# Performance work log

Hardware: AMD Instinct MI355X
Metric: run time of the kernel (lower is better)

The kernel has to match this reference:

```python
import jax, jax.numpy as jnp
import numpy as np

B, C, HW = 128, 3, 224
P = 16
D = 256
NH = 8
HD = D // NH
E = 4            # num_experts
K = 2            # top-k
FF = 4 * D
NC = 38
EPS = 1e-5


def _layernorm(x, g, b):
    mu = jnp.mean(x, axis=-1, keepdims=True)
    var = jnp.mean(jnp.square(x - mu), axis=-1, keepdims=True)
    return (x - mu) * jax.lax.rsqrt(var + EPS) * g + b


def setup_inputs() -> dict:
    key = jax.random.key(0)
    ks = jax.random.split(key, 16)
    s = 0.02
    return {
        "x": jax.random.normal(ks[0], (B, C, HW, HW), dtype=jnp.float32),
        "conv_w": jax.random.normal(ks[1], (D, C, P, P), dtype=jnp.float32) * s,
        "conv_b": jnp.zeros((D,), jnp.float32),
        "cls_token": jnp.zeros((1, 1, D), jnp.float32),
        "ln1_g": jnp.ones((D,), jnp.float32),
        "ln1_b": jnp.zeros((D,), jnp.float32),
        "qkv_w": jax.random.normal(ks[2], (3 * D, D), dtype=jnp.float32) * s,
        "qkv_b": jnp.zeros((3 * D,), jnp.float32),
        "out_w": jax.random.normal(ks[3], (D, D), dtype=jnp.float32) * s,
        "out_b": jnp.zeros((D,), jnp.float32),
        "ln2_g": jnp.ones((D,), jnp.float32),
        "ln2_b": jnp.zeros((D,), jnp.float32),
        "router_w": jax.random.normal(ks[4], (E, D), dtype=jnp.float32) * s,
        "router_b": jnp.zeros((E,), jnp.float32),
        "e_w1": jax.random.normal(ks[5], (E, D, FF), dtype=jnp.float32) * s,
        "e_b1": jnp.zeros((E, FF), jnp.float32),
        "e_w2": jax.random.normal(ks[6], (E, FF, D), dtype=jnp.float32) * s,
        "e_b2": jnp.zeros((E, D), jnp.float32),
        "head_w": jax.random.normal(ks[7], (NC, D), dtype=jnp.float32) * s,
        "head_b": jnp.zeros((NC,), jnp.float32),
    }


def reference(x, conv_w, conv_b, cls_token, ln1_g, ln1_b, qkv_w, qkv_b,
              out_w, out_b, ln2_g, ln2_b, router_w, router_b,
              e_w1, e_b1, e_w2, e_b2, head_w, head_b):
    # patch embed: Conv2d(3, D, 16, 16) -> [B, D, 14, 14] -> [B, 196, D]
    h = jax.lax.conv_general_dilated(
        x, conv_w, window_strides=(P, P), padding="VALID",
        dimension_numbers=("NCHW", "OIHW", "NCHW")) + conv_b[None, :, None, None]
    b = h.shape[0]
    tok = h.reshape(b, D, -1).transpose(0, 2, 1)            # [B, 196, D]
    tok = jnp.concatenate([jnp.broadcast_to(cls_token, (b, 1, D)), tok], axis=1)  # [B, 197, D]
    S = tok.shape[1]

    # Multi-head self-attention (pre-norm)
    x2 = _layernorm(tok, ln1_g, ln1_b)
    qkv = x2 @ qkv_w.T + qkv_b                              # [B, S, 3D]
    q, k, v = jnp.split(qkv, 3, axis=-1)
    q = q.reshape(b, S, NH, HD)
    k = k.reshape(b, S, NH, HD)
    v = v.reshape(b, S, NH, HD)
    scores = jnp.einsum("bqhd,bkhd->bhqk", q, k) / np.float32(np.sqrt(HD))
    attn = jax.nn.softmax(scores, axis=-1)
    ao = jnp.einsum("bhqk,bkhd->bqhd", attn, v).reshape(b, S, D)
    ao = ao @ out_w.T + out_b
    tok = tok + ao

    # MoE FFN (pre-norm). NOTE: original code computes top-k routing weights
    # but never multiplies outputs by them — outputs of selected experts are
    # simply summed. We reproduce that faithfully.
    x2 = _layernorm(tok, ln2_g, ln2_b)
    x_flat = x2.reshape(-1, D)                              # [T, D]
    logits = x_flat @ router_w.T + router_b                 # [T, E]
    probs = jax.nn.softmax(logits, axis=-1)
    _topw, topi = jax.lax.top_k(probs, K)                   # topw unused (as in source)
    mask = (topi[..., None] == jnp.arange(E)).any(axis=1)   # [T, E] bool
    out_flat = jnp.zeros_like(x_flat)
    for i in range(E):                                       # fixed small expert count
        hid = jax.nn.gelu(x_flat @ e_w1[i] + e_b1[i], approximate=False)
        out_flat = out_flat + mask[:, i:i + 1].astype(x_flat.dtype) * (hid @ e_w2[i] + e_b2[i])
    tok = tok + out_flat.reshape(b, S, D)

    return tok[:, 0] @ head_w.T + head_b                    # [B, NC]
```

## Files before the change

### kernel.cpp

```cpp
#include <hip/hip_runtime.h>
#include <hip/hip_bf16.h>
#include <math.h>

#define TTOK   25216
#define SEQL   197
#define NBATCH 128
#define DMODEL 256
#define NHEADS 8
#define FFD    1024
#define NEXP   4
#define NCLS   38
#define CONVK  768
#define NPATCH 196
#define CM     25088

typedef unsigned short u16;
typedef unsigned int u32;
using s16x8 = __attribute__((ext_vector_type(8))) short;
using f32x4 = __attribute__((ext_vector_type(4))) float;

__device__ __forceinline__ float b2f(u16 v) {
  union { unsigned u; float f; } x; x.u = (unsigned)v << 16; return x.f;
}
__device__ __forceinline__ u16 f2b(float f) {
  __hip_bfloat16 h = __float2bfloat16(f);
  return *reinterpret_cast<u16*>(&h);
}
__device__ __forceinline__ void gload16(const void* g, void* l) {
  __builtin_amdgcn_global_load_lds(
      (const __attribute__((address_space(1))) void*)g,
      (__attribute__((address_space(3))) void*)l, 16, 0, 0);
}
__device__ __forceinline__ float warp_sum(float v) {
  #pragma unroll
  for (int o = 32; o; o >>= 1) v += __shfl_xor(v, o);
  return v;
}
__device__ __forceinline__ float warp_max(float v) {
  #pragma unroll
  for (int o = 32; o; o >>= 1) v = fmaxf(v, __shfl_xor(v, o));
  return v;
}
__device__ __forceinline__ int fsw(int row) { return (row ^ (row >> 2)) & 3; }

__global__ __launch_bounds__(256) void k_cast2(const float* __restrict__ in,
                                               u16* __restrict__ hi,
                                               u16* __restrict__ lo) {
  int i = (blockIdx.x * 256 + threadIdx.x) * 4;
  float4 v = *(const float4*)&in[i];
  float vv[4] = {v.x, v.y, v.z, v.w};
  u16 h[4], l[4];
  #pragma unroll
  for (int j = 0; j < 4; ++j) {
    h[j] = f2b(vv[j]);
    l[j] = f2b(vv[j] - b2f(h[j]));
  }
  *(uint2*)&hi[i] = *(const uint2*)h;
  *(uint2*)&lo[i] = *(const uint2*)l;
}

__global__ __launch_bounds__(256) void k_conv(const float* __restrict__ x,
                                              const u16* __restrict__ cwh,
                                              const u16* __restrict__ cwl,
                                              const float* __restrict__ cb,
                                              float* __restrict__ tok) {
  const int m0 = blockIdx.x * 128;
  const int n0 = blockIdx.y * 128;
  __shared__ __align__(16) u16 lds[4 * 128 * 32];
  u16* Ah_s = lds;
  u16* Al_s = lds + 4096;
  u16* Wh_s = lds + 8192;
  u16* Wl_s = lds + 12288;
  const int tid = threadIdx.x;
  const int lane = tid & 63;
  const int wv = tid >> 6;
  const int wr = wv >> 1, wc = wv & 1;
  const int l15 = lane & 15, l4 = lane >> 4;
  f32x4 acc[4][4] = {};

  const int kk_t = (tid & 7) * 4;
  long abase[4]; int aldso[4];
  #pragma unroll
  for (int it = 0; it < 4; ++it) {
    int row = it * 32 + (tid >> 3);
    int m = m0 + row;
    int b = m / NPATCH, p = m - b * NPATCH;
    int py = p / 14, px = p - py * 14;
    abase[it] = (long)(b * 3) * 50176 + (py * 16) * 224 + px * 16;
    aldso[it] = row * 64 + (((kk_t >> 3) ^ fsw(row)) << 4) + (kk_t & 7) * 2;
  }
  long woff[2]; int wofs[2];
  #pragma unroll
  for (int r = 0; r < 2; ++r) {
    int off = r * 4096 + tid * 16;
    int row = off >> 6;
    int c16 = (off >> 4) & 3;
    int kk = (c16 ^ fsw(row)) << 3;
    woff[r] = (long)(n0 + row) * CONVK + kk;
    wofs[r] = off;
  }
  for (int kc = 0; kc < CONVK; kc += 32) {
    #pragma unroll
    for (int r = 0; r < 2; ++r) {
      gload16(cwh + woff[r] + kc, (char*)Wh_s + wofs[r]);
      gload16(cwl + woff[r] + kc, (char*)Wl_s + wofs[r]);
    }
    int k = kc + kk_t;
    int c = k >> 8, r8 = k & 255;
    long soff = (long)c * 50176 + (r8 >> 4) * 224 + (r8 & 15);
    #pragma unroll
    for (int it = 0; it < 4; ++it) {
      float4 v = *(const float4*)&x[abase[it] + soff];
      float vv[4] = {v.x, v.y, v.z, v.w};
      u16 h[4], l[4];
      #pragma unroll
      for (int j = 0; j < 4; ++j) {
        h[j] = f2b(vv[j]);
        l[j] = f2b(vv[j] - b2f(h[j]));
      }
      *(uint2*)((char*)Ah_s + aldso[it]) = *(const uint2*)h;
      *(uint2*)((char*)Al_s + aldso[it]) = *(const uint2*)l;
    }
    __syncthreads();
    s16x8 ah[4], al[4], bh[4], bl[4];
    #pragma unroll
    for (int i = 0; i < 4; ++i) {
      int rowa = wr * 64 + i * 16 + l15;
      int kba = (l4 ^ fsw(rowa)) << 4;
      ah[i] = *(const s16x8*)((const char*)Ah_s + rowa * 64 + kba);
      al[i] = *(const s16x8*)((const char*)Al_s + rowa * 64 + kba);
      int rowb = wc * 64 + i * 16 + l15;
      int kbb = (l4 ^ fsw(rowb)) << 4;
      bh[i] = *(const s16x8*)((const char*)Wh_s + rowb * 64 + kbb);
      bl[i] = *(const s16x8*)((const char*)Wl_s + rowb * 64 + kbb);
    }
    #pragma unroll
    for (int i = 0; i < 4; ++i)
      #pragma unroll
      for (int j = 0; j < 4; ++j)
        acc[i][j] = __builtin_amdgcn_mfma_f32_16x16x32_bf16(ah[i], bh[j],
                                                            acc[i][j], 0, 0, 0);
    #pragma unroll
    for (int i = 0; i < 4; ++i)
      #pragma unroll
      for (int j = 0; j < 4; ++j)
        acc[i][j] = __builtin_amdgcn_mfma_f32_16x16x32_bf16(ah[i], bl[j],
                                                            acc[i][j], 0, 0, 0);
    #pragma unroll
    for (int i = 0; i < 4; ++i)
      #pragma unroll
      for (int j = 0; j < 4; ++j)
        acc[i][j] = __builtin_amdgcn_mfma_f32_16x16x32_bf16(al[i], bh[j],
                                                            acc[i][j], 0, 0, 0);
    __syncthreads();
  }
  const int mb = m0 + wr * 64 + (l4 << 2);
  const int nb = n0 + wc * 64 + l15;
  #pragma unroll
  for (int i = 0; i < 4; ++i) {
    #pragma unroll
    for (int jf = 0; jf < 4; ++jf) {
      #pragma unroll
      for (int j = 0; j < 4; ++j) {
        int m = mb + i * 16 + j;
        int n = nb + jf * 16;
        int bq = m / NPATCH;
        long cr = (long)bq * SEQL + (m - bq * NPATCH) + 1;
        tok[cr * DMODEL + n] = acc[i][jf][j] + cb[n];
      }
    }
  }
}

__global__ __launch_bounds__(256) void k_qkv(const u16* __restrict__ Ah,
                                             const u16* __restrict__ Al,
                                             const u16* __restrict__ Wh,
                                             const u16* __restrict__ Wl,
                                             const float* __restrict__ bias,
                                             float* __restrict__ Cf) {
  const int m0 = blockIdx.x * 128;
  const int n0 = blockIdx.y * 128;
  const int K = DMODEL, ldc = 512;
  __shared__ __align__(16) u16 lds[4 * 128 * 32];
  u16* Ah_s = lds;
  u16* Al_s = lds + 4096;
  u16* Wh_s = lds + 8192;
  u16* Wl_s = lds + 12288;
  const int tid = threadIdx.x;
  const int lane = tid & 63;
  const int wv = tid >> 6;
  const int wr = wv >> 1, wc = wv & 1;
  const int l15 = lane & 15, l4 = lane >> 4;
  f32x4 acc[4][4] = {};

  long aoff[2], woff[2]; int ofs[2];
  #pragma unroll
  for (int r = 0; r < 2; ++r) {
    int off = r * 4096 + tid * 16;
    int row = off >> 6;
    int c16 = (off >> 4) & 3;
    int kk = (c16 ^ fsw(row)) << 3;
    aoff[r] = (long)(m0 + row) * K + kk;
    woff[r] = (long)(n0 + row) * K + kk;
    ofs[r] = off;
  }
  for (int kc = 0; kc < K; kc += 32) {
    #pragma unroll
    for (int r = 0; r < 2; ++r) {
      gload16(Ah + aoff[r] + kc, (char*)Ah_s + ofs[r]);
      gload16(Al + aoff[r] + kc, (char*)Al_s + ofs[r]);
      gload16(Wh + woff[r] + kc, (char*)Wh_s + ofs[r]);
      gload16(Wl + woff[r] + kc, (char*)Wl_s + ofs[r]);
    }
    __syncthreads();
    s16x8 ah[4], al[4], bh[4], bl[4];
    #pragma unroll
    for (int i = 0; i < 4; ++i) {
      int rowa = wr * 64 + i * 16 + l15;
      int kba = (l4 ^ fsw(rowa)) << 4;
      ah[i] = *(const s16x8*)((const char*)Ah_s + rowa * 64 + kba);
      al[i] = *(const s16x8*)((const char*)Al_s + rowa * 64 + kba);
      int rowb = wc * 64 + i * 16 + l15;
      int kbb = (l4 ^ fsw(rowb)) << 4;
      bh[i] = *(const s16x8*)((const char*)Wh_s + rowb * 64 + kbb);
      bl[i] = *(const s16x8*)((const char*)Wl_s + rowb * 64 + kbb);
    }
    #pragma unroll
    for (int i = 0; i < 4; ++i)
      #pragma unroll
      for (int j = 0; j < 4; ++j)
        acc[i][j] = __builtin_amdgcn_mfma_f32_16x16x32_bf16(ah[i], bh[j],
                                                            acc[i][j], 0, 0, 0);
    #pragma unroll
    for (int i = 0; i < 4; ++i)
      #pragma unroll
      for (int j = 0; j < 4; ++j)
        acc[i][j] = __builtin_amdgcn_mfma_f32_16x16x32_bf16(ah[i], bl[j],
                                                            acc[i][j], 0, 0, 0);
    #pragma unroll
    for (int i = 0; i < 4; ++i)
      #pragma unroll
      for (int j = 0; j < 4; ++j)
        acc[i][j] = __builtin_amdgcn_mfma_f32_16x16x32_bf16(al[i], bh[j],
                                                            acc[i][j], 0, 0, 0);
    __syncthreads();
  }
  const int mb = m0 + wr * 64 + (l4 << 2);
  const int nb = n0 + wc * 64 + l15;
  #pragma unroll
  for (int i = 0; i < 4; ++i) {
    #pragma unroll
    for (int jf = 0; jf < 4; ++jf) {
      #pragma unroll
      for (int j = 0; j < 4; ++j) {
        int m = mb + i * 16 + j;
        int n = nb + jf * 16;
        Cf[(long)m * ldc + n] = acc[i][jf][j] + bias[n];
      }
    }
  }
}

__global__ __launch_bounds__(256) void k_ln4(const float* __restrict__ in,
                                             u16* __restrict__ outh,
                                             u16* __restrict__ outl,
                                             const float* __restrict__ g,
                                             const float* __restrict__ bb) {
  const int row = blockIdx.x * 4 + (threadIdx.x >> 6);
  const int lane = threadIdx.x & 63;
  float vv[4];
  *(float4*)vv = *(const float4*)&in[(size_t)row * DMODEL + lane * 4];
  float s1 = vv[0] + vv[1] + vv[2] + vv[3];
  float s2 = vv[0]*vv[0] + vv[1]*vv[1] + vv[2]*vv[2] + vv[3]*vv[3];
  s1 = warp_sum(s1);
  s2 = warp_sum(s2);
  float mu = s1 * (1.f / DMODEL);
  float var = s2 * (1.f / DMODEL) - mu * mu;
  float rs = rsqrtf(var + 1e-5f);
  u16 hh[4], ll[4];
  #pragma unroll
  for (int j = 0; j < 4; ++j) {
    float r = (vv[j] - mu) * rs * g[lane * 4 + j] + bb[lane * 4 + j];
    hh[j] = f2b(r);
    ll[j] = f2b(r - b2f(hh[j]));
  }
  *(uint2*)&outh[(size_t)row * DMODEL + lane * 4] = *(const uint2*)hh;
  *(uint2*)&outl[(size_t)row * DMODEL + lane * 4] = *(const uint2*)ll;
}

__global__ void k_cls(const float* __restrict__ cls, float* __restrict__ tok) {
  tok[(size_t)blockIdx.x * SEQL * DMODEL + threadIdx.x] = cls[threadIdx.x];
}

__global__ __launch_bounds__(256) void k_qcls(const u16* __restrict__ x2h,
                                              const u16* __restrict__ x2l,
                                              const u16* __restrict__ qwh,
                                              const u16* __restrict__ qwl,
                                              const float* __restrict__ qb,
                                              u16* __restrict__ qch,
                                              u16* __restrict__ qcl) {
  const int b = blockIdx.x, n = threadIdx.x;
  __shared__ float xs[DMODEL];
  size_t r0 = (size_t)b * SEQL * DMODEL;
  xs[n] = b2f(x2h[r0 + n]) + b2f(x2l[r0 + n]);
  __syncthreads();
  float val = qb[n];
  #pragma unroll 4
  for (int i = 0; i < 32; ++i) {
    s16x8 wh = *(const s16x8*)(qwh + (size_t)n * DMODEL + i * 8);
    s16x8 wl = *(const s16x8*)(qwl + (size_t)n * DMODEL + i * 8);
    #pragma unroll
    for (int j = 0; j < 8; ++j)
      val = fmaf(b2f((u16)wh[j]) + b2f((u16)wl[j]), xs[i * 8 + j], val);
  }
  u16 h = f2b(val);
  qch[b * DMODEL + n] = h;
  qcl[b * DMODEL + n] = f2b(val - b2f(h));
}

__global__ __launch_bounds__(256) void k_attn_cls(const u16* __restrict__ qch,
                                                  const u16* __restrict__ qcl,
                                                  const float* __restrict__ kvf,
                                                  float* __restrict__ ao) {
  const int w = threadIdx.x >> 6, lane = threadIdx.x & 63;
  const int unit = blockIdx.x * 4 + w;
  const int b = unit >> 3, h = unit & 7;
  __shared__ float Ss[4][200];
  float q[32];
  #pragma unroll
  for (int i = 0; i < 4; ++i) {
    s16x8 vh = *(const s16x8*)(qch + b * DMODEL + h * 32 + i * 8);
    s16x8 vl = *(const s16x8*)(qcl + b * DMODEL + h * 32 + i * 8);
    #pragma unroll
    for (int j = 0; j < 8; ++j) q[i * 8 + j] = b2f((u16)vh[j]) + b2f((u16)vl[j]);
  }
  float sc[4];
  float mx = -1e30f;
  #pragma unroll
  for (int r = 0; r < 4; ++r) {
    int k = lane + 64 * r;
    float s = -1e30f;
    if (k < SEQL) {
      const float* kr = kvf + ((size_t)(b * SEQL + k)) * 512 + h * 32;
      s = 0.f;
      #pragma unroll
      for (int i = 0; i < 8; ++i) {
        float4 kv4 = *(const float4*)(kr + i * 4);
        s = fmaf(kv4.x, q[i * 4 + 0], s);
        s = fmaf(kv4.y, q[i * 4 + 1], s);
        s = fmaf(kv4.z, q[i * 4 + 2], s);
        s = fmaf(kv4.w, q[i * 4 + 3], s);
      }
      s *= 0.17677669529663687f;
    }
    sc[r] = s;
    mx = fmaxf(mx, s);
  }
  mx = warp_max(mx);
  float sm = 0.f;
  #pragma unroll
  for (int r = 0; r < 4; ++r) {
    int k = lane + 64 * r;
    float e = (k < SEQL) ? __expf(sc[r] - mx) : 0.f;
    sc[r] = e;
    sm += e;
  }
  sm = warp_sum(sm);
  float inv = 1.f / sm;
  #pragma unroll
  for (int r = 0; r < 4; ++r) {
    int k = lane + 64 * r;
    if (k < SEQL) Ss[w][k] = sc[r] * inv;
  }
  int d = lane & 31, half = lane >> 5;
  float acc = 0.f;
  for (int i = 0; i < 99; ++i) {
    int k = half * 99 + i;
    if (k < SEQL)
      acc = fmaf(Ss[w][k], kvf[((size_t)(b * SEQL + k)) * 512 + 256 + h * 32 + d], acc);
  }
  acc += __shfl_xor(acc, 32);
  if (lane < 32) ao[(b * NHEADS + h) * 32 + d] = acc;
}

__global__ __launch_bounds__(256) void k_oproj_route(
    const float* __restrict__ ao, const float* __restrict__ ow,
    const float* __restrict__ ob, const float* __restrict__ tok,
    const float* __restrict__ g, const float* __restrict__ bb,
    const float* __restrict__ rw, const float* __restrict__ rb,
    float* __restrict__ tokc, float* __restrict__ x2cf,
    float* __restrict__ maskf) {
  const int b = blockIdx.x, n = threadIdx.x;
  const int w = n >> 6, lane = n & 63;
  __shared__ float xs[DMODEL];
  __shared__ float xd_s[DMODEL];
  __shared__ float red[8];
  __shared__ float lg[4];
  xs[n] = ao[b * DMODEL + n];
  __syncthreads();
  float val = ob[n];
  #pragma unroll 4
  for (int i = 0; i < 64; ++i) {
    float4 wv = *(const float4*)(ow + (size_t)n * DMODEL + i * 4);
    val = fmaf(wv.x, xs[i * 4 + 0], val);
    val = fmaf(wv.y, xs[i * 4 + 1], val);
    val = fmaf(wv.z, xs[i * 4 + 2], val);
    val = fmaf(wv.w, xs[i * 4 + 3], val);
  }
  float t = tok[(size_t)b * SEQL * DMODEL + n] + val;
  tokc[b * DMODEL + n] = t;
  float s1 = warp_sum(t), s2 = warp_sum(t * t);
  if (lane == 0) { red[w] = s1; red[4 + w] = s2; }
  __syncthreads();
  s1 = red[0] + red[1] + red[2] + red[3];
  s2 = red[4] + red[5] + red[6] + red[7];
  float mu = s1 * (1.f / DMODEL);
  float var = s2 * (1.f / DMODEL) - mu * mu;
  float rs = rsqrtf(var + 1e-5f);
  float xd = (t - mu) * rs * g[n] + bb[n];
  x2cf[b * DMODEL + n] = xd;
  xd_s[n] = xd;
  __syncthreads();
  float s = 0.f;
  #pragma unroll
  for (int i = 0; i < 4; ++i) s = fmaf(xd_s[lane + i * 64], rw[w * DMODEL + lane + i * 64], s);
  s = warp_sum(s) + rb[w];
  if (lane == 0) lg[w] = s;
  __syncthreads();
  if (n < NEXP) {
    int e = n;
    int rank = 0;
    #pragma unroll
    for (int j = 0; j < NEXP; ++j)
      if (j != e && (lg[j] > lg[e] || (lg[j] == lg[e] && j < e))) ++rank;
    maskf[b * NEXP + e] = (rank < 2) ? 1.f : 0.f;
  }
}

__global__ __launch_bounds__(256) void k_moe1(const float* __restrict__ x2cf,
                                              const float* __restrict__ w1,
                                              const float* __restrict__ b1,
                                              const float* __restrict__ maskf,
                                              float* __restrict__ hid) {
  const int e = blockIdx.x, t = blockIdx.y;
  if (maskf[t * NEXP + e] == 0.f) return;
  __shared__ float xs[DMODEL];
  const int tid = threadIdx.x;
  xs[tid] = x2cf[t * DMODEL + tid];
  __syncthreads();
  const float* w1e = w1 + (size_t)e * DMODEL * FFD + tid;
  float a0 = 0.f, a1 = 0.f, a2 = 0.f, a3 = 0.f;
  #pragma unroll 4
  for (int k = 0; k < DMODEL; ++k) {
    float xv = xs[k];
    const float* wr_ = w1e + (size_t)k * FFD;
    a0 = fmaf(xv, wr_[0], a0);
    a1 = fmaf(xv, wr_[256], a1);
    a2 = fmaf(xv, wr_[512], a2);
    a3 = fmaf(xv, wr_[768], a3);
  }
  float accs[4] = {a0, a1, a2, a3};
  float* hrow = hid + ((size_t)e * NBATCH + t) * FFD;
  #pragma unroll
  for (int j = 0; j < 4; ++j) {
    float v = accs[j] + b1[e * FFD + tid + j * 256];
    hrow[tid + j * 256] = 0.5f * v * (1.0f + erff(v * 0.70710678118654752f));
  }
}

__global__ __launch_bounds__(256) void k_moe2(const float* __restrict__ hid,
                                              const float* __restrict__ w2,
                                              const float* __restrict__ b2,
                                              const float* __restrict__ maskf,
                                              float* __restrict__ tokc) {
  const int t = blockIdx.x, dc = blockIdx.y;
  const int tid = threadIdx.x;
  const int dl = tid & 127, kh = tid >> 7;
  const int dout = dc * 128 + dl;
  int e0 = 0;
  while (e0 < 3 && maskf[t * NEXP + e0] == 0.f) ++e0;
  int e1 = e0 + 1;
  while (e1 < 3 && maskf[t * NEXP + e1] == 0.f) ++e1;
  __shared__ float hs0[FFD], hs1[FFD];
  const float* h0 = hid + ((size_t)e0 * NBATCH + t) * FFD;
  const float* h1 = hid + ((size_t)e1 * NBATCH + t) * FFD;
  for (int i = tid * 4; i < FFD; i += 1024) {
    *(float4*)&hs0[i] = *(const float4*)&h0[i];
    *(float4*)&hs1[i] = *(const float4*)&h1[i];
  }
  __syncthreads();
  const float* w20 = w2 + (size_t)e0 * FFD * DMODEL + dout;
  const float* w21 = w2 + (size_t)e1 * FFD * DMODEL + dout;
  float a0 = 0.f, a1 = 0.f;
  const int k0 = kh * 512;
  #pragma unroll 8
  for (int k = k0; k < k0 + 512; ++k) {
    a0 = fmaf(hs0[k], w20[(size_t)k * DMODEL], a0);
    a1 = fmaf(hs1[k], w21[(size_t)k * DMODEL], a1);
  }
  __shared__ float red[256];
  red[tid] = a0 + a1;
  __syncthreads();
  if (kh == 0) {
    float full = red[dl] + red[128 + dl] +
                 b2[e0 * DMODEL + dout] + b2[e1 * DMODEL + dout];
    tokc[t * DMODEL + dout] += full;
  }
}

__global__ __launch_bounds__(256) void k_head(const float* __restrict__ tokc,
                                              const float* __restrict__ hw,
                                              const float* __restrict__ hb,
                                              float* __restrict__ out) {
  int b = blockIdx.x;
  int w = threadIdx.x >> 6, lane = threadIdx.x & 63;
  const float* row = tokc + (size_t)b * DMODEL;
  for (int c = w; c < NCLS; c += 4) {
    float s = 0.f;
    for (int d = lane; d < DMODEL; d += 64) s = fmaf(row[d], hw[c * DMODEL + d], s);
    s = warp_sum(s);
    if (lane == 0) out[b * NCLS + c] = s + hb[c];
  }
}

extern "C" void kernel_launch(void* const* d_in, const int* in_sizes, int n_in,
                              void* d_out, int out_size, void* d_ws, size_t ws_size,
                              hipStream_t stream) {
  const float* x      = (const float*)d_in[0];
  const float* conv_w = (const float*)d_in[1];
  const float* conv_b = (const float*)d_in[2];
  const float* cls    = (const float*)d_in[3];
  const float* ln1g   = (const float*)d_in[4];
  const float* ln1b   = (const float*)d_in[5];
  const float* qkv_w  = (const float*)d_in[6];
  const float* qkv_b  = (const float*)d_in[7];
  const float* out_w  = (const float*)d_in[8];
  const float* out_b  = (const float*)d_in[9];
  const float* ln2g   = (const float*)d_in[10];
  const float* ln2b   = (const float*)d_in[11];
  const float* rw     = (const float*)d_in[12];
  const float* rb     = (const float*)d_in[13];
  const float* e_w1   = (const float*)d_in[14];
  const float* e_b1   = (const float*)d_in[15];
  const float* e_w2   = (const float*)d_in[16];
  const float* e_b2   = (const float*)d_in[17];
  const float* head_w = (const float*)d_in[18];
  const float* head_b = (const float*)d_in[19];
  float* out = (float*)d_out;

  char* ws = (char*)d_ws;
  size_t off = 0;
  auto alloc = [&](size_t bytes) {
    void* p = ws + off;
    off += (bytes + 255) & ~(size_t)255;
    return p;
  };
  float* tok   = (float*)alloc((size_t)TTOK * DMODEL * 4);
  u16*   x2h   = (u16*)alloc((size_t)TTOK * DMODEL * 2);
  u16*   x2l   = (u16*)alloc((size_t)TTOK * DMODEL * 2);
  float* qkvf  = (float*)alloc((size_t)TTOK * 512 * 4);
  u16*   cwh   = (u16*)alloc((size_t)DMODEL * CONVK * 2);
  u16*   cwl   = (u16*)alloc((size_t)DMODEL * CONVK * 2);
  u16*   qwh   = (u16*)alloc((size_t)768 * DMODEL * 2);
  u16*   qwl   = (u16*)alloc((size_t)768 * DMODEL * 2);
  u16*   qch   = (u16*)alloc((size_t)NBATCH * DMODEL * 2);
  u16*   qcl   = (u16*)alloc((size_t)NBATCH * DMODEL * 2);
  float* aocf  = (float*)alloc((size_t)NBATCH * DMODEL * 4);
  float* tokc  = (float*)alloc((size_t)NBATCH * DMODEL * 4);
  float* x2cf  = (float*)alloc((size_t)NBATCH * DMODEL * 4);
  float* maskf = (float*)alloc((size_t)NBATCH * NEXP * 4);
  float* hid   = (float*)alloc((size_t)NEXP * NBATCH * FFD * 4);

  k_cast2<<<192, 256, 0, stream>>>(conv_w, cwh, cwl);
  k_cast2<<<192, 256, 0, stream>>>(qkv_w, qwh, qwl);

  k_conv<<<dim3(CM / 128, 2), 256, 0, stream>>>(x, cwh, cwl, conv_b, tok);
  k_cls<<<NBATCH, DMODEL, 0, stream>>>(cls, tok);

  k_ln4<<<TTOK / 4, 256, 0, stream>>>(tok, x2h, x2l, ln1g, ln1b);

  k_qkv<<<dim3(TTOK / 128, 4), 256, 0, stream>>>(
      x2h, x2l, qwh + 256 * DMODEL, qwl + 256 * DMODEL, qkv_b + 256, qkvf);

  k_qcls<<<NBATCH, 256, 0, stream>>>(x2h, x2l, qwh, qwl, qkv_b, qch, qcl);

  k_attn_cls<<<NBATCH * NHEADS / 4, 256, 0, stream>>>(qch, qcl, qkvf, aocf);

  k_oproj_route<<<NBATCH, 256, 0, stream>>>(aocf, out_w, out_b, tok,
                                            ln2g, ln2b, rw, rb,
                                            tokc, x2cf, maskf);

  k_moe1<<<dim3(NEXP, NBATCH), 256, 0, stream>>>(x2cf, e_w1, e_b1, maskf, hid);
  k_moe2<<<dim3(NBATCH, 2), 256, 0, stream>>>(hid, e_w2, e_b2, maskf, tokc);

  k_head<<<NBATCH, 256, 0, stream>>>(tokc, head_w, head_b, out);
}
```

Baseline: 212.3 us.

## Fuse LayerNorm apply into QKV GEMM A-load and retile conv GEMM

The LayerNorm kernel that wrote bf16 hi/lo copies of the normalized activations is replaced by a stats-only kernel. The QKV GEMM now reads fp32 tokens directly, normalizes them, and splits them into hi/lo while staging A into padded LDS. This removes a full write and re-read of two activation arrays. The conv GEMM is also retiled to 64-row M tiles with N-major grid ordering so more blocks run and weight tiles are shared, and both kernels use padded (80-byte stride) LDS rows instead of swizzled layout for A.

```diff
diff --git a/kernel.cpp b/kernel.cpp
--- a/kernel.cpp
+++ b/kernel.cpp
@@ -64,30 +64,30 @@
                                               const u16* __restrict__ cwl,
                                               const float* __restrict__ cb,
                                               float* __restrict__ tok) {
-  const int m0 = blockIdx.x * 128;
-  const int n0 = blockIdx.y * 128;
-  __shared__ __align__(16) u16 lds[4 * 128 * 32];
+  const int n0 = blockIdx.x * 128;
+  const int m0 = blockIdx.y * 64;
+  __shared__ __align__(16) u16 lds[2 * 64 * 40 + 2 * 128 * 32];
   u16* Ah_s = lds;
-  u16* Al_s = lds + 4096;
-  u16* Wh_s = lds + 8192;
-  u16* Wl_s = lds + 12288;
+  u16* Al_s = lds + 64 * 40;
+  u16* Wh_s = lds + 2 * 64 * 40;
+  u16* Wl_s = lds + 2 * 64 * 40 + 128 * 32;
   const int tid = threadIdx.x;
   const int lane = tid & 63;
   const int wv = tid >> 6;
   const int wr = wv >> 1, wc = wv & 1;
   const int l15 = lane & 15, l4 = lane >> 4;
-  f32x4 acc[4][4] = {};
-
-  const int kk_t = (tid & 7) * 4;
-  long abase[4]; int aldso[4];
-  #pragma unroll
-  for (int it = 0; it < 4; ++it) {
+  f32x4 acc[2][4] = {};
+
+  const int kpos = (tid & 7) * 4;
+  long abase[2]; int aldso[2];
+  #pragma unroll
+  for (int it = 0; it < 2; ++it) {
     int row = it * 32 + (tid >> 3);
     int m = m0 + row;
     int b = m / NPATCH, p = m - b * NPATCH;
     int py = p / 14, px = p - py * 14;
     abase[it] = (long)(b * 3) * 50176 + (py * 16) * 224 + px * 16;
-    aldso[it] = row * 64 + (((kk_t >> 3) ^ fsw(row)) << 4) + (kk_t & 7) * 2;
+    aldso[it] = row * 80 + kpos * 2;
   }
   long woff[2]; int wofs[2];
   #pragma unroll
@@ -105,11 +105,11 @@
       gload16(cwh + woff[r] + kc, (char*)Wh_s + wofs[r]);
       gload16(cwl + woff[r] + kc, (char*)Wl_s + wofs[r]);
     }
-    int k = kc + kk_t;
+    int k = kc + kpos;
     int c = k >> 8, r8 = k & 255;
     long soff = (long)c * 50176 + (r8 >> 4) * 224 + (r8 & 15);
     #pragma unroll
-    for (int it = 0; it < 4; ++it) {
+    for (int it = 0; it < 2; ++it) {
       float4 v = *(const float4*)&x[abase[it] + soff];
       float vv[4] = {v.x, v.y, v.z, v.w};
       u16 h[4], l[4];
@@ -122,42 +122,44 @@
       *(uint2*)((char*)Al_s + aldso[it]) = *(const uint2*)l;
     }
     __syncthreads();
-    s16x8 ah[4], al[4], bh[4], bl[4];
-    #pragma unroll
-    for (int i = 0; i < 4; ++i) {
-      int rowa = wr * 64 + i * 16 + l15;
-      int kba = (l4 ^ fsw(rowa)) << 4;
-      ah[i] = *(const s16x8*)((const char*)Ah_s + rowa * 64 + kba);
-      al[i] = *(const s16x8*)((const char*)Al_s + rowa * 64 + kba);
-      int rowb = wc * 64 + i * 16 + l15;
+    s16x8 ah[2], al[2], bh[4], bl[4];
+    #pragma unroll
+    for (int i = 0; i < 2; ++i) {
+      int rowa = wr * 32 + i * 16 + l15;
+      ah[i] = *(const s16x8*)((const char*)Ah_s + rowa * 80 + l4 * 16);
+      al[i] = *(const s16x8*)((const char*)Al_s + rowa * 80 + l4 * 16);
+    }
+    #pragma unroll
+    for (int j = 0; j < 4; ++j) {
+      int rowb = wc * 64 + j * 16 + l15;
       int kbb = (l4 ^ fsw(rowb)) << 4;
-      bh[i] = *(const s16x8*)((const char*)Wh_s + rowb * 64 + kbb);
-      bl[i] = *(const s16x8*)((const char*)Wl_s + rowb * 64 + kbb);
-    }
-    #pragma unroll
-    for (int i = 0; i < 4; ++i)
+      bh[j] = *(const s16x8*)((const char*)Wh_s + rowb * 64 + kbb);
+      bl[j] = *(const s16x8*)((const char*)Wl_s + rowb * 64 + kbb);
+    }
+    #pragma unroll
+    for (int i = 0; i < 2; ++i)
       #pragma unroll
       for (int j = 0; j < 4; ++j)
         acc[i][j] = __builtin_amdgcn_mfma_f32_16x16x32_bf16(ah[i], bh[j],
                                                             acc[i][j], 0, 0, 0);
     #pragma unroll
-    for (int i = 0; i < 4; ++i)
+    for (int i = 0; i < 2; ++i)
       #pragma unroll
       for (int j = 0; j < 4; ++j)
         acc[i][j] = __builtin_amdgcn_mfma_f32_16x16x32_bf16(ah[i], bl[j],
                                                             acc[i][j], 0, 0, 0);
     #pragma unroll
-    for (int i = 0; i < 4; ++i)
+    for (int i = 0; i < 2; ++i)
       #pragma unroll
       for (int j = 0; j < 4; ++j)
         acc[i][j] = __builtin_amdgcn_mfma_f32_16x16x32_bf16(al[i], bh[j],
                                                             acc[i][j], 0, 0, 0);
     __syncthreads();
   }
-  const int mb = m0 + wr * 64 + (l4 << 2);
+  const int mb = m0 + wr * 32 + (l4 << 2);
   const int nb = n0 + wc * 64 + l15;
   #pragma unroll
-  for (int i = 0; i < 4; ++i) {
+  for (int i = 0; i < 2; ++i) {
     #pragma unroll
     for (int jf = 0; jf < 4; ++jf) {
       #pragma unroll
@@ -172,20 +174,37 @@
   }
 }
 
-__global__ __launch_bounds__(256) void k_qkv(const u16* __restrict__ Ah,
-                                             const u16* __restrict__ Al,
+__global__ __launch_bounds__(256) void k_lnstat(const float* __restrict__ in,
+                                                float2* __restrict__ st) {
+  const int row = blockIdx.x * 4 + (threadIdx.x >> 6);
+  const int lane = threadIdx.x & 63;
+  float4 v = *(const float4*)&in[(size_t)row * DMODEL + lane * 4];
+  float s1 = v.x + v.y + v.z + v.w;
+  float s2 = v.x * v.x + v.y * v.y + v.z * v.z + v.w * v.w;
+  s1 = warp_sum(s1);
+  s2 = warp_sum(s2);
+  if (lane == 0) {
+    float mu = s1 * (1.f / DMODEL);
+    float var = s2 * (1.f / DMODEL) - mu * mu;
+    st[row] = make_float2(mu, rsqrtf(var + 1e-5f));
+  }
+}
+
+__global__ __launch_bounds__(256) void k_qkv(const float* __restrict__ tok,
+                                             const float2* __restrict__ stats,
+                                             const float* __restrict__ g,
+                                             const float* __restrict__ bb,
                                              const u16* __restrict__ Wh,
                                              const u16* __restrict__ Wl,
                                              const float* __restrict__ bias,
                                              float* __restrict__ Cf) {
-  const int m0 = blockIdx.x * 128;
-  const int n0 = blockIdx.y * 128;
-  const int K = DMODEL, ldc = 512;
-  __shared__ __align__(16) u16 lds[4 * 128 * 32];
+  const int n0 = blockIdx.x * 128;
+  const int m0 = blockIdx.y * 128;
+  __shared__ __align__(16) u16 lds[2 * 128 * 40 + 2 * 128 * 32];
   u16* Ah_s = lds;
-  u16* Al_s = lds + 4096;
-  u16* Wh_s = lds + 8192;
-  u16* Wl_s = lds + 12288;
+  u16* Al_s = lds + 128 * 40;
+  u16* Wh_s = lds + 2 * 128 * 40;
+  u16* Wl_s = lds + 2 * 128 * 40 + 128 * 32;
   const int tid = threadIdx.x;
   const int lane = tid & 63;
   const int wv = tid >> 6;
@@ -193,33 +212,57 @@
   const int l15 = lane & 15, l4 = lane >> 4;
   f32x4 acc[4][4] = {};
 
-  long aoff[2], woff[2]; int ofs[2];
+  const int kpos = (tid & 7) * 4;
+  long atok[4]; float2 st[4]; int aldso[4];
+  #pragma unroll
+  for (int it = 0; it < 4; ++it) {
+    int row = it * 32 + (tid >> 3);
+    int m = m0 + row;
+    atok[it] = (long)m * DMODEL;
+    st[it] = stats[m];
+    aldso[it] = row * 80 + kpos * 2;
+  }
+  long woff[2]; int wofs[2];
   #pragma unroll
   for (int r = 0; r < 2; ++r) {
     int off = r * 4096 + tid * 16;
     int row = off >> 6;
     int c16 = (off >> 4) & 3;
     int kk = (c16 ^ fsw(row)) << 3;
-    aoff[r] = (long)(m0 + row) * K + kk;
-    woff[r] = (long)(n0 + row) * K + kk;
-    ofs[r] = off;
-  }
-  for (int kc = 0; kc < K; kc += 32) {
+    woff[r] = (long)(n0 + row) * DMODEL + kk;
+    wofs[r] = off;
+  }
+  for (int kc = 0; kc < DMODEL; kc += 32) {
     #pragma unroll
     for (int r = 0; r < 2; ++r) {
-      gload16(Ah + aoff[r] + kc, (char*)Ah_s + ofs[r]);
-      gload16(Al + aoff[r] + kc, (char*)Al_s + ofs[r]);
-      gload16(Wh + woff[r] + kc, (char*)Wh_s + ofs[r]);
-      gload16(Wl + woff[r] + kc, (char*)Wl_s + ofs[r]);
+      gload16(Wh + woff[r] + kc, (char*)Wh_s + wofs[r]);
+      gload16(Wl + woff[r] + kc, (char*)Wl_s + wofs[r]);
+    }
+    float4 g4 = *(const float4*)&g[kc + kpos];
+    float4 b4 = *(const float4*)&bb[kc + kpos];
+    float gg[4] = {g4.x, g4.y, g4.z, g4.w};
+    float bbv[4] = {b4.x, b4.y, b4.z, b4.w};
+    #pragma unroll
+    for (int it = 0; it < 4; ++it) {
+      float4 v = *(const float4*)&tok[atok[it] + kc + kpos];
+      float vv[4] = {v.x, v.y, v.z, v.w};
+      u16 h[4], l[4];
+      #pragma unroll
+      for (int j = 0; j < 4; ++j) {
+        float xd = (vv[j] - st[it].x) * st[it].y * gg[j] + bbv[j];
+        h[j] = f2b(xd);
+        l[j] = f2b(xd - b2f(h[j]));
+      }
+      *(uint2*)((char*)Ah_s + aldso[it]) = *(const uint2*)h;
+      *(uint2*)((char*)Al_s + aldso[it]) = *(const uint2*)l;
     }
     __syncthreads();
     s16x8 ah[4], al[4], bh[4], bl[4];
     #pragma unroll
     for (int i = 0; i < 4; ++i) {
       int rowa = wr * 64 + i * 16 + l15;
-      int kba = (l4 ^ fsw(rowa)) << 4;
-      ah[i] = *(const s16x8*)((const char*)Ah_s + rowa * 64 + kba);
-      al[i] = *(const s16x8*)((const char*)Al_s + rowa * 64 + kba);
+      ah[i] = *(const s16x8*)((const char*)Ah_s + rowa * 80 + l4 * 16);
+      al[i] = *(const s16x8*)((const char*)Al_s + rowa * 80 + l4 * 16);
       int rowb = wc * 64 + i * 16 + l15;
       int kbb = (l4 ^ fsw(rowb)) << 4;
       bh[i] = *(const s16x8*)((const char*)Wh_s + rowb * 64 + kbb);
@@ -255,45 +298,20 @@
       for (int j = 0; j < 4; ++j) {
         int m = mb + i * 16 + j;
         int n = nb + jf * 16;
-        Cf[(long)m * ldc + n] = acc[i][jf][j] + bias[n];
+        Cf[(long)m * 512 + n] = acc[i][jf][j] + bias[n];
       }
     }
   }
-}
-
-__global__ __launch_bounds__(256) void k_ln4(const float* __restrict__ in,
-                                             u16* __restrict__ outh,
-                                             u16* __restrict__ outl,
-                                             const float* __restrict__ g,
-                                             const float* __restrict__ bb) {
-  const int row = blockIdx.x * 4 + (threadIdx.x >> 6);
-  const int lane = threadIdx.x & 63;
-  float vv[4];
-  *(float4*)vv = *(const float4*)&in[(size_t)row * DMODEL + lane * 4];
-  float s1 = vv[0] + vv[1] + vv[2] + vv[3];
-  float s2 = vv[0]*vv[0] + vv[1]*vv[1] + vv[2]*vv[2] + vv[3]*vv[3];
-  s1 = warp_sum(s1);
-  s2 = warp_sum(s2);
-  float mu = s1 * (1.f / DMODEL);
-  float var = s2 * (1.f / DMODEL) - mu * mu;
-  float rs = rsqrtf(var + 1e-5f);
-  u16 hh[4], ll[4];
-  #pragma unroll
-  for (int j = 0; j < 4; ++j) {
-    float r = (vv[j] - mu) * rs * g[lane * 4 + j] + bb[lane * 4 + j];
-    hh[j] = f2b(r);
-    ll[j] = f2b(r - b2f(hh[j]));
-  }
-  *(uint2*)&outh[(size_t)row * DMODEL + lane * 4] = *(const uint2*)hh;
-  *(uint2*)&outl[(size_t)row * DMODEL + lane * 4] = *(const uint2*)ll;
 }
 
 __global__ void k_cls(const float* __restrict__ cls, float* __restrict__ tok) {
   tok[(size_t)blockIdx.x * SEQL * DMODEL + threadIdx.x] = cls[threadIdx.x];
 }
 
-__global__ __launch_bounds__(256) void k_qcls(const u16* __restrict__ x2h,
-                                              const u16* __restrict__ x2l,
+__global__ __launch_bounds__(256) void k_qcls(const float* __restrict__ tok,
+                                              const float2* __restrict__ stats,
+                                              const float* __restrict__ g,
+                                              const float* __restrict__ bb,
                                               const u16* __restrict__ qwh,
                                               const u16* __restrict__ qwl,
                                               const float* __restrict__ qb,
@@ -301,8 +319,9 @@
                                               u16* __restrict__ qcl) {
   const int b = blockIdx.x, n = threadIdx.x;
   __shared__ float xs[DMODEL];
-  size_t r0 = (size_t)b * SEQL * DMODEL;
-  xs[n] = b2f(x2h[r0 + n]) + b2f(x2l[r0 + n]);
+  float2 st = stats[b * SEQL];
+  float v = tok[(size_t)b * SEQL * DMODEL + n];
+  xs[n] = (v - st.x) * st.y * g[n] + bb[n];
   __syncthreads();
   float val = qb[n];
   #pragma unroll 4
@@ -555,34 +574,35 @@
     off += (bytes + 255) & ~(size_t)255;
     return p;
   };
-  float* tok   = (float*)alloc((size_t)TTOK * DMODEL * 4);
-  u16*   x2h   = (u16*)alloc((size_t)TTOK * DMODEL * 2);
-  u16*   x2l   = (u16*)alloc((size_t)TTOK * DMODEL * 2);
-  float* qkvf  = (float*)alloc((size_t)TTOK * 512 * 4);
-  u16*   cwh   = (u16*)alloc((size_t)DMODEL * CONVK * 2);
-  u16*   cwl   = (u16*)alloc((size_t)DMODEL * CONVK * 2);
-  u16*   qwh   = (u16*)alloc((size_t)768 * DMODEL * 2);
-  u16*   qwl   = (u16*)alloc((size_t)768 * DMODEL * 2);
-  u16*   qch   = (u16*)alloc((size_t)NBATCH * DMODEL * 2);
-  u16*   qcl   = (u16*)alloc((size_t)NBATCH * DMODEL * 2);
-  float* aocf  = (float*)alloc((size_t)NBATCH * DMODEL * 4);
-  float* tokc  = (float*)alloc((size_t)NBATCH * DMODEL * 4);
-  float* x2cf  = (float*)alloc((size_t)NBATCH * DMODEL * 4);
-  float* maskf = (float*)alloc((size_t)NBATCH * NEXP * 4);
-  float* hid   = (float*)alloc((size_t)NEXP * NBATCH * FFD * 4);
+  float*  tok   = (float*)alloc((size_t)TTOK * DMODEL * 4);
+  float*  qkvf  = (float*)alloc((size_t)TTOK * 512 * 4);
+  float2* stats = (float2*)alloc((size_t)TTOK * 8);
+  u16*    cwh   = (u16*)alloc((size_t)DMODEL * CONVK * 2);
+  u16*    cwl   = (u16*)alloc((size_t)DMODEL * CONVK * 2);
+  u16*    qwh   = (u16*)alloc((size_t)768 * DMODEL * 2);
+  u16*    qwl   = (u16*)alloc((size_t)768 * DMODEL * 2);
+  u16*    qch   = (u16*)alloc((size_t)NBATCH * DMODEL * 2);
+  u16*    qcl   = (u16*)alloc((size_t)NBATCH * DMODEL * 2);
+  float*  aocf  = (float*)alloc((size_t)NBATCH * DMODEL * 4);
+  float*  tokc  = (float*)alloc((size_t)NBATCH * DMODEL * 4);
+  float*  x2cf  = (float*)alloc((size_t)NBATCH * DMODEL * 4);
+  float*  maskf = (float*)alloc((size_t)NBATCH * NEXP * 4);
+  float*  hid   = (float*)alloc((size_t)NEXP * NBATCH * FFD * 4);
 
   k_cast2<<<192, 256, 0, stream>>>(conv_w, cwh, cwl);
   k_cast2<<<192, 256, 0, stream>>>(qkv_w, qwh, qwl);
 
-  k_conv<<<dim3(CM / 128, 2), 256, 0, stream>>>(x, cwh, cwl, conv_b, tok);
+  k_conv<<<dim3(2, CM / 64), 256, 0, stream>>>(x, cwh, cwl, conv_b, tok);
   k_cls<<<NBATCH, DMODEL, 0, stream>>>(cls, tok);
 
-  k_ln4<<<TTOK / 4, 256, 0, stream>>>(tok, x2h, x2l, ln1g, ln1b);
-
-  k_qkv<<<dim3(TTOK / 128, 4), 256, 0, stream>>>(
-      x2h, x2l, qwh + 256 * DMODEL, qwl + 256 * DMODEL, qkv_b + 256, qkvf);
-
-  k_qcls<<<NBATCH, 256, 0, stream>>>(x2h, x2l, qwh, qwl, qkv_b, qch, qcl);
+  k_lnstat<<<TTOK / 4, 256, 0, stream>>>(tok, stats);
+
+  k_qkv<<<dim3(4, TTOK / 128), 256, 0, stream>>>(
+      tok, stats, ln1g, ln1b, qwh + 256 * DMODEL, qwl + 256 * DMODEL,
+      qkv_b + 256, qkvf);
+
+  k_qcls<<<NBATCH, 256, 0, stream>>>(tok, stats, ln1g, ln1b, qwh, qwl, qkv_b,
+                                     qch, qcl);
 
   k_attn_cls<<<NBATCH * NHEADS / 4, 256, 0, stream>>>(qch, qcl, qkvf, aocf);
 
```

Measured after the change: 212.9 us. No clear change (+0.3%).
